# Kernel optimization log

Measured on AMD Instinct MI355X. Metric: run time of the kernel, lower is better.

The kernel has to match this reference:

```python
import jax, jax.numpy as jnp
import numpy as np

# Static per-expert capacities (tokens are laid out contiguously per expert)
CAPS = [1024, 512, 1024, 256, 1024, 512, 128, 1024, 512, 1024, 256, 512, 1024, 128, 64, 512]
TOTAL = sum(CAPS)  # 9536
E, H, I = 16, 1024, 4096
OFFSETS = np.concatenate([[0], np.cumsum(CAPS)])


def setup_inputs() -> dict:
    key = jax.random.key(0)
    ks = jax.random.split(key, 5)
    x = jax.random.normal(ks[0], (TOTAL, H), dtype=jnp.float32)
    W1 = jax.random.normal(ks[1], (E, I, H), dtype=jnp.float32) * 0.02
    b1 = jax.random.normal(ks[2], (E, I), dtype=jnp.float32) * 0.02
    W2 = jax.random.normal(ks[3], (E, H, I), dtype=jnp.float32) * 0.02
    b2 = jax.random.normal(ks[4], (E, H), dtype=jnp.float32) * 0.02
    return {"x": x, "W1": W1, "b1": b1, "W2": W2, "b2": b2}


def reference(x, W1, b1, W2, b2):
    # Grouped GEMM FFN: expert e processes rows [OFFSETS[e]:OFFSETS[e+1]]
    # out = gelu(x_e @ W1[e].T + b1[e]) @ W2[e].T + b2[e]
    outs = []
    for e in range(E):  # fixed, static loop over experts (capacities are static)
        xs = x[OFFSETS[e]:OFFSETS[e + 1]]                      # [cap_e, H]
        h = jax.nn.gelu(xs @ W1[e].T + b1[e], approximate=False)  # [cap_e, I]
        outs.append(h @ W2[e].T + b2[e])                       # [cap_e, H]
    return jnp.concatenate(outs, axis=0)                       # [TOTAL, H]
```

## Files before the change

kernel.cpp:

```cpp
#include <hip/hip_runtime.h>
#include <math.h>

typedef __attribute__((ext_vector_type(8))) short short8;
typedef __attribute__((ext_vector_type(4))) float f32x4;
typedef __attribute__((ext_vector_type(2))) unsigned int u32x2;

#define E_NUM 16
constexpr int CAPS[E_NUM] = {1024,512,1024,256,1024,512,128,1024,512,1024,256,512,1024,128,64,512};
constexpr int OFFS[E_NUM] = {0,1024,1536,2560,2816,3840,4352,4480,5504,6016,7040,7296,7808,8832,8960,9024};
constexpr int cdiv_(int a, int b){ return (a + b - 1) / b; }
constexpr int ilog2_(int v){ int l = 0; while ((1 << l) < v) ++l; return l; }

__device__ __forceinline__ unsigned int cvt_pk_bf16(float a, float b){
  unsigned int r;
  asm("v_cvt_pk_bf16_f32 %0, %1, %2" : "=v"(r) : "v"(a), "v"(b));
  return r;
}

typedef __attribute__((address_space(1))) const unsigned char gas_u8;
typedef __attribute__((address_space(3))) unsigned char las_u8;
__device__ __forceinline__ void gl_lds16(const void* g, void* l){
  __builtin_amdgcn_global_load_lds((gas_u8*)g, (las_u8*)l, 16, 0, 0);
}

__global__ __launch_bounds__(256) void cvt_bf16_kernel(const float* __restrict__ x,
                                                       unsigned short* __restrict__ xb, int n8)
{
  int i = blockIdx.x * blockDim.x + threadIdx.x;
  const int stride = gridDim.x * blockDim.x;
  for (; i < n8; i += stride) {
    f32x4 a = *reinterpret_cast<const f32x4*>(x + (size_t)i * 8);
    f32x4 b = *reinterpret_cast<const f32x4*>(x + (size_t)i * 8 + 4);
    u32x2 lo, hi;
    lo[0] = cvt_pk_bf16(a[0], a[1]); lo[1] = cvt_pk_bf16(a[2], a[3]);
    hi[0] = cvt_pk_bf16(b[0], b[1]); hi[1] = cvt_pk_bf16(b[2], b[3]);
    *reinterpret_cast<u32x2*>(xb + (size_t)i * 8)     = lo;
    *reinterpret_cast<u32x2*>(xb + (size_t)i * 8 + 4) = hi;
  }
}

template<bool A_GLDS, bool GELU_OUT, int TM, int NDIM, int KDIM, int LOG_GN, int NWG, int KS>
__global__ __launch_bounds__(256, 8)
void expert_gemm(const void* __restrict__ Av, const float* __restrict__ W,
                 const float* __restrict__ bias, void* __restrict__ Outv)
{
  constexpr int A_SZ = TM * 32;
  constexpr int B_SZ = 128 * 32;
  constexpr int GN   = 1 << LOG_GN;
  constexpr int MFR  = TM / 32;
  constexpr int NT   = KDIM / (KS * 32);
  constexpr int NWG1 = NWG / KS;
  static_assert(NWG % 8 == 0, "grid must be divisible by 8 for XCD swizzle");
  static_assert(!GELU_OUT || 2 * (A_SZ + B_SZ) >= 128 * 128, "GELU transpose needs 32KB");
  static_assert(!GELU_OUT || KS == 1, "GELU path is KS=1 only");

  __shared__ __align__(16) unsigned short smem[2 * A_SZ + 2 * B_SZ];

  const int tid  = threadIdx.x;
  const int braw = blockIdx.x;
  const int t = (braw & 7) * (NWG / 8) + (braw >> 3);

  const int kc    = t / NWG1;
  const int tt    = t % NWG1;
  const int kbase = kc * (KDIM / KS);

  int m0 = 0, n0 = 0, Me = 0, tok0 = 0;
  size_t wbase = 0, bbase = 0;
  {
    int acc0 = 0;
    #pragma unroll
    for (int i = 0; i < E_NUM; ++i) {
      const int mt  = cdiv_(CAPS[i], TM);
      const int lmt = ilog2_(mt);
      const int nb  = mt * (NDIM / 128);
      if (tt >= acc0 && tt < acc0 + nb) {
        const int loc = tt - acc0;
        const int g   = loc >> (lmt + LOG_GN);
        const int rem = loc & ((mt << LOG_GN) - 1);
        m0   = (rem >> LOG_GN) * TM;
        n0   = ((g << LOG_GN) | (rem & (GN - 1))) * 128;
        Me   = CAPS[i];
        tok0 = OFFS[i];
        wbase = (size_t)i * NDIM * KDIM;
        bbase = (size_t)i * NDIM;
      }
      acc0 += nb;
    }
  }
  const float* Wb = W + wbase;

  const int lane = tid & 63;
  const int wv   = tid >> 6;
  const int sr   = tid >> 3;
  const int sc   = (tid & 7) * 8;
  const int spc  = sc ^ (((sr >> 2) & 3) << 4);

  const unsigned short* Ah = (const unsigned short*)Av;
  const float*          Af = (const float*)Av;

  f32x4 ra[MFR]; f32x4 rb[4];

  auto loadB = [&](int kt) {
    const int k0 = kbase + kt * 32;
    #pragma unroll
    for (int i = 0; i < 4; ++i)
      rb[i] = *reinterpret_cast<const f32x4*>(Wb + (size_t)(n0 + sr + 32 * i) * KDIM + k0 + (sc >> 1));
  };
  auto writeB = [&](int buf) {
    char* bb = (char*)(smem + 2 * A_SZ + buf * B_SZ);
    #pragma unroll
    for (int i = 0; i < 4; ++i) {
      u32x2 p;
      p[0] = cvt_pk_bf16(rb[i][0], rb[i][1]);
      p[1] = cvt_pk_bf16(rb[i][2], rb[i][3]);
      *reinterpret_cast<u32x2*>(bb + (sr + 32 * i) * 64 + spc) = p;
    }
  };

  auto stageA_glds = [&](int buf, int kt) {
    constexpr int AI = TM / 64;
    const unsigned short* Ag = Ah + (size_t)(tok0 + m0) * KDIM + kbase + kt * 32;
    #pragma unroll
    for (int j = 0; j < AI; ++j) {
      const int rbase = wv * (AI * 16) + j * 16;
      const int r     = rbase + (lane >> 2);
      const int gblk  = (lane & 3) ^ ((r >> 2) & 3);
      gl_lds16((const void*)(Ag + (size_t)r * KDIM + gblk * 8),
               (void*)(smem + buf * A_SZ + rbase * 32));
    }
  };
  auto loadA_reg = [&](int kt) {
    const int k0 = kbase + kt * 32;
    #pragma unroll
    for (int i = 0; i < MFR; ++i)
      ra[i] = *reinterpret_cast<const f32x4*>(Af + (size_t)(tok0 + m0 + sr + 32 * i) * KDIM + k0 + (sc >> 1));
  };
  auto writeA_reg = [&](int buf) {
    char* ab = (char*)(smem + buf * A_SZ);
    #pragma unroll
    for (int i = 0; i < MFR; ++i) {
      u32x2 p;
      p[0] = cvt_pk_bf16(ra[i][0], ra[i][1]);
      p[1] = cvt_pk_bf16(ra[i][2], ra[i][3]);
      *reinterpret_cast<u32x2*>(ab + (sr + 32 * i) * 64 + spc) = p;
    }
  };

  const int wm   = (wv >> 1) * (TM / 2);
  const int wn   = (wv & 1) * 64;
  const int lrow = lane & 15;
  const int fcs  = ((lane >> 4) << 4) ^ (((lane >> 2) & 3) << 4);

  f32x4 acc_[MFR][4];
  #pragma unroll
  for (int i = 0; i < MFR; ++i)
    #pragma unroll
    for (int j = 0; j < 4; ++j)
      acc_[i][j] = (f32x4){0.f, 0.f, 0.f, 0.f};

  auto mfma_step = [&](int cur) {
    const char* ab = (const char*)(smem + cur * A_SZ);
    const char* bb = (const char*)(smem + 2 * A_SZ + cur * B_SZ);
    short8 afr[MFR], bfr[4];
    #pragma unroll
    for (int f = 0; f < MFR; ++f)
      afr[f] = *reinterpret_cast<const short8*>(ab + (wm + f * 16 + lrow) * 64 + fcs);
    #pragma unroll
    for (int f = 0; f < 4; ++f)
      bfr[f] = *reinterpret_cast<const short8*>(bb + (wn + f * 16 + lrow) * 64 + fcs);
    #pragma unroll
    for (int i = 0; i < MFR; ++i)
      #pragma unroll
      for (int j = 0; j < 4; ++j)
        acc_[i][j] = __builtin_amdgcn_mfma_f32_16x16x32_bf16(afr[i], bfr[j], acc_[i][j], 0, 0, 0);
  };

  loadB(0);
  if constexpr (A_GLDS) stageA_glds(0, 0); else loadA_reg(0);
  writeB(0);
  if constexpr (!A_GLDS) writeA_reg(0);
  __syncthreads();

  for (int kt = 0; kt < NT; ++kt) {
    const int cur = kt & 1;
    if (kt + 1 < NT) {
      loadB(kt + 1);
      if constexpr (A_GLDS) stageA_glds(cur ^ 1, kt + 1);
      else                  loadA_reg(kt + 1);
    }
    mfma_step(cur);
    if (kt + 1 < NT) {
      writeB(cur ^ 1);
      if constexpr (!A_GLDS) writeA_reg(cur ^ 1);
    }
    __syncthreads();
  }

  float bv[4];
  #pragma unroll
  for (int f = 0; f < 4; ++f)
    bv[f] = bias[bbase + n0 + wn + f * 16 + lrow];

  if constexpr (GELU_OUT) {
    static_assert(TM == 128, "GELU path assumes 128-row tiles");
    unsigned short* hout = smem;
    #pragma unroll
    for (int i = 0; i < MFR; ++i) {
      const int rbase = wm + i * 16 + (lane >> 4) * 4;
      #pragma unroll
      for (int j = 0; j < 4; ++j) {
        #pragma unroll
        for (int jj = 0; jj < 4; ++jj) {
          float xv = acc_[i][j][jj] + bv[j];
          float y2 = xv * (1.5957691216057308f + 0.07135481627f * xv * xv);
          float g  = xv * __builtin_amdgcn_rcpf(1.0f + __expf(-y2));
          hout[(rbase + jj) * 128 + wn + j * 16 + lrow] = (unsigned short)(cvt_pk_bf16(g, g) & 0xFFFFu);
        }
      }
    }
    __syncthreads();
    unsigned short* Oh = (unsigned short*)Outv;
    #pragma unroll
    for (int it = 0; it < 8; ++it) {
      int row  = it * 16 + (tid >> 4);
      int c    = (tid & 15) * 8;
      int grow = m0 + row;
      if (grow < Me) {
        *reinterpret_cast<short8*>(Oh + (size_t)(tok0 + grow) * NDIM + n0 + c)
          = *reinterpret_cast<const short8*>(hout + row * 128 + c);
      }
    }
  } else {
    float* Of = (float*)Outv;
    constexpr float BS = 1.0f / (float)KS;
    #pragma unroll
    for (int i = 0; i < MFR; ++i) {
      const int rbase = wm + i * 16 + (lane >> 4) * 4;
      #pragma unroll
      for (int jj = 0; jj < 4; ++jj) {
        int grow = m0 + rbase + jj;
        if (grow < Me) {
          #pragma unroll
          for (int j = 0; j < 4; ++j) {
            float v = acc_[i][j][jj] + bv[j] * BS;
            float* p = Of + (size_t)(tok0 + grow) * NDIM + n0 + wn + j * 16 + lrow;
            if constexpr (KS > 1) unsafeAtomicAdd(p, v);
            else                  *p = v;
          }
        }
      }
    }
  }
}

extern "C" void kernel_launch(void* const* d_in, const int* in_sizes, int n_in,
                              void* d_out, int out_size, void* d_ws, size_t ws_size,
                              hipStream_t stream)
{
  const float* x  = (const float*)d_in[0];
  const float* W1 = (const float*)d_in[1];
  const float* b1 = (const float*)d_in[2];
  const float* W2 = (const float*)d_in[3];
  const float* b2 = (const float*)d_in[4];
  float* out = (float*)d_out;

  constexpr size_t H_BYTES  = (size_t)9536 * 4096 * 2;
  constexpr size_t XB_BYTES = (size_t)9536 * 1024 * 2;
  unsigned short* h  = (unsigned short*)d_ws;
  unsigned short* xb = (unsigned short*)((char*)d_ws + H_BYTES);

  const bool use_xb = ws_size >= H_BYTES + XB_BYTES;

  hipMemsetAsync(d_out, 0, (size_t)out_size * sizeof(float), stream);

  if (use_xb) {
    cvt_bf16_kernel<<<2048, 256, 0, stream>>>(x, xb, 9536 * 1024 / 8);
    expert_gemm<true, true, 128, 4096, 1024, 2, 75 * 32, 1>
        <<<75 * 32, 256, 0, stream>>>((const void*)xb, W1, b1, (void*)h);
  } else {
    expert_gemm<false, true, 128, 4096, 1024, 2, 75 * 32, 1>
        <<<75 * 32, 256, 0, stream>>>((const void*)x, W1, b1, (void*)h);
  }

  expert_gemm<true, false, 128, 1024, 4096, 0, 2 * 75 * 8, 2>
      <<<2 * 75 * 8, 256, 0, stream>>>((const void*)h, W2, b2, (void*)out);
}
```

Measured before the change: 367.2 us.

## Stage fp32 weights directly to LDS and convert to bf16 at fragment load

Weight tiles are now copied from global memory into LDS as raw fp32 using the direct global-to-LDS load path, instead of being loaded into registers, converted to bf16 and written to LDS. Conversion to bf16 moves into the MFMA fragment read, with a new XOR swizzle for both A and B tiles. This frees registers and removes the register round-trip and its stalls. In exchange the B tile in LDS doubles in size, LDS reads per step double, the conversion is repeated by each wave reading the same tile, and the occupancy hint drops from 8 to 3 blocks.

Result: no change. 371.6 us (+1.2%).

```diff
diff --git a/kernel.cpp b/kernel.cpp
--- a/kernel.cpp
+++ b/kernel.cpp
@@ -4,6 +4,7 @@
 typedef __attribute__((ext_vector_type(8))) short short8;
 typedef __attribute__((ext_vector_type(4))) float f32x4;
 typedef __attribute__((ext_vector_type(2))) unsigned int u32x2;
+typedef __attribute__((ext_vector_type(4))) unsigned int u32x4;
 
 #define E_NUM 16
 constexpr int CAPS[E_NUM] = {1024,512,1024,256,1024,512,128,1024,512,1024,256,512,1024,128,64,512};
@@ -40,21 +41,21 @@
 }
 
 template<bool A_GLDS, bool GELU_OUT, int TM, int NDIM, int KDIM, int LOG_GN, int NWG, int KS>
-__global__ __launch_bounds__(256, 8)
+__global__ __launch_bounds__(256, 3)
 void expert_gemm(const void* __restrict__ Av, const float* __restrict__ W,
                  const float* __restrict__ bias, void* __restrict__ Outv)
 {
-  constexpr int A_SZ = TM * 32;
-  constexpr int B_SZ = 128 * 32;
+  constexpr int A_BYTES = TM * 64;
+  constexpr int B_BYTES = 128 * 128;
   constexpr int GN   = 1 << LOG_GN;
   constexpr int MFR  = TM / 32;
   constexpr int NT   = KDIM / (KS * 32);
   constexpr int NWG1 = NWG / KS;
   static_assert(NWG % 8 == 0, "grid must be divisible by 8 for XCD swizzle");
-  static_assert(!GELU_OUT || 2 * (A_SZ + B_SZ) >= 128 * 128, "GELU transpose needs 32KB");
+  static_assert(!GELU_OUT || (2 * A_BYTES + 2 * B_BYTES) >= 128 * 128 * 2, "GELU needs 32KB");
   static_assert(!GELU_OUT || KS == 1, "GELU path is KS=1 only");
 
-  __shared__ __align__(16) unsigned short smem[2 * A_SZ + 2 * B_SZ];
+  __shared__ __align__(16) char smem[2 * A_BYTES + 2 * B_BYTES];
 
   const int tid  = threadIdx.x;
   const int braw = blockIdx.x;
@@ -91,44 +92,37 @@
 
   const int lane = tid & 63;
   const int wv   = tid >> 6;
-  const int sr   = tid >> 3;
-  const int sc   = (tid & 7) * 8;
-  const int spc  = sc ^ (((sr >> 2) & 3) << 4);
 
   const unsigned short* Ah = (const unsigned short*)Av;
   const float*          Af = (const float*)Av;
 
-  f32x4 ra[MFR]; f32x4 rb[4];
-
-  auto loadB = [&](int kt) {
-    const int k0 = kbase + kt * 32;
-    #pragma unroll
-    for (int i = 0; i < 4; ++i)
-      rb[i] = *reinterpret_cast<const f32x4*>(Wb + (size_t)(n0 + sr + 32 * i) * KDIM + k0 + (sc >> 1));
-  };
-  auto writeB = [&](int buf) {
-    char* bb = (char*)(smem + 2 * A_SZ + buf * B_SZ);
-    #pragma unroll
-    for (int i = 0; i < 4; ++i) {
-      u32x2 p;
-      p[0] = cvt_pk_bf16(rb[i][0], rb[i][1]);
-      p[1] = cvt_pk_bf16(rb[i][2], rb[i][3]);
-      *reinterpret_cast<u32x2*>(bb + (sr + 32 * i) * 64 + spc) = p;
-    }
-  };
-
-  auto stageA_glds = [&](int buf, int kt) {
-    constexpr int AI = TM / 64;
+  auto stageB = [&](int buf, int kt) {
+    const float* Bg = Wb + (size_t)n0 * KDIM + kbase + kt * 32;
+    char* dst0 = smem + 2 * A_BYTES + buf * B_BYTES;
+    #pragma unroll
+    for (int j = 0; j < 4; ++j) {
+      const int rbase = wv * 32 + j * 8;
+      const int r     = rbase + (lane >> 3);
+      const int lblk  = (lane & 7) ^ (r & 7);
+      gl_lds16((const void*)(Bg + (size_t)r * KDIM + lblk * 4), (void*)(dst0 + rbase * 128));
+    }
+  };
+
+  auto stageA = [&](int buf, int kt) {
     const unsigned short* Ag = Ah + (size_t)(tok0 + m0) * KDIM + kbase + kt * 32;
-    #pragma unroll
-    for (int j = 0; j < AI; ++j) {
-      const int rbase = wv * (AI * 16) + j * 16;
+    char* dst0 = smem + buf * A_BYTES;
+    #pragma unroll
+    for (int j = 0; j < TM / 64; ++j) {
+      const int rbase = wv * (TM / 4) + j * 16;
       const int r     = rbase + (lane >> 2);
-      const int gblk  = (lane & 3) ^ ((r >> 2) & 3);
-      gl_lds16((const void*)(Ag + (size_t)r * KDIM + gblk * 8),
-               (void*)(smem + buf * A_SZ + rbase * 32));
-    }
-  };
+      const int lblk  = (lane & 3) ^ (r & 3);
+      gl_lds16((const void*)(Ag + (size_t)r * KDIM + lblk * 8), (void*)(dst0 + rbase * 64));
+    }
+  };
+
+  const int sr = tid >> 3;
+  const int sc = (tid & 7) * 8;
+  f32x4 ra[MFR];
   auto loadA_reg = [&](int kt) {
     const int k0 = kbase + kt * 32;
     #pragma unroll
@@ -136,20 +130,21 @@
       ra[i] = *reinterpret_cast<const f32x4*>(Af + (size_t)(tok0 + m0 + sr + 32 * i) * KDIM + k0 + (sc >> 1));
   };
   auto writeA_reg = [&](int buf) {
-    char* ab = (char*)(smem + buf * A_SZ);
+    char* ab = smem + buf * A_BYTES;
     #pragma unroll
     for (int i = 0; i < MFR; ++i) {
       u32x2 p;
       p[0] = cvt_pk_bf16(ra[i][0], ra[i][1]);
       p[1] = cvt_pk_bf16(ra[i][2], ra[i][3]);
-      *reinterpret_cast<u32x2*>(ab + (sr + 32 * i) * 64 + spc) = p;
+      *reinterpret_cast<u32x2*>(ab + (sr + 32 * i) * 64 + (sc ^ ((sr & 3) << 4))) = p;
     }
   };
 
   const int wm   = (wv >> 1) * (TM / 2);
   const int wn   = (wv & 1) * 64;
   const int lrow = lane & 15;
-  const int fcs  = ((lane >> 4) << 4) ^ (((lane >> 2) & 3) << 4);
+  const int pa0  = (((lane >> 4) ^ (lane & 3)) << 4);
+  const int pb0  = ((((lane >> 4) << 1) ^ (lane & 7)) << 4);
 
   f32x4 acc_[MFR][4];
   #pragma unroll
@@ -159,15 +154,24 @@
       acc_[i][j] = (f32x4){0.f, 0.f, 0.f, 0.f};
 
   auto mfma_step = [&](int cur) {
-    const char* ab = (const char*)(smem + cur * A_SZ);
-    const char* bb = (const char*)(smem + 2 * A_SZ + cur * B_SZ);
+    const char* ab  = smem + cur * A_BYTES;
+    const char* bbp = smem + 2 * A_BYTES + cur * B_BYTES;
     short8 afr[MFR], bfr[4];
     #pragma unroll
     for (int f = 0; f < MFR; ++f)
-      afr[f] = *reinterpret_cast<const short8*>(ab + (wm + f * 16 + lrow) * 64 + fcs);
-    #pragma unroll
-    for (int f = 0; f < 4; ++f)
-      bfr[f] = *reinterpret_cast<const short8*>(bb + (wn + f * 16 + lrow) * 64 + fcs);
+      afr[f] = *reinterpret_cast<const short8*>(ab + (wm + f * 16 + lrow) * 64 + pa0);
+    #pragma unroll
+    for (int f = 0; f < 4; ++f) {
+      const char* rowp = bbp + (size_t)(wn + f * 16 + lrow) * 128;
+      f32x4 lo = *reinterpret_cast<const f32x4*>(rowp + pb0);
+      f32x4 hi = *reinterpret_cast<const f32x4*>(rowp + (pb0 ^ 16));
+      u32x4 pk;
+      pk[0] = cvt_pk_bf16(lo[0], lo[1]);
+      pk[1] = cvt_pk_bf16(lo[2], lo[3]);
+      pk[2] = cvt_pk_bf16(hi[0], hi[1]);
+      pk[3] = cvt_pk_bf16(hi[2], hi[3]);
+      bfr[f] = __builtin_bit_cast(short8, pk);
+    }
     #pragma unroll
     for (int i = 0; i < MFR; ++i)
       #pragma unroll
@@ -175,24 +179,19 @@
         acc_[i][j] = __builtin_amdgcn_mfma_f32_16x16x32_bf16(afr[i], bfr[j], acc_[i][j], 0, 0, 0);
   };
 
-  loadB(0);
-  if constexpr (A_GLDS) stageA_glds(0, 0); else loadA_reg(0);
-  writeB(0);
-  if constexpr (!A_GLDS) writeA_reg(0);
+  if constexpr (A_GLDS) stageA(0, 0); else { loadA_reg(0); writeA_reg(0); }
+  stageB(0, 0);
   __syncthreads();
 
   for (int kt = 0; kt < NT; ++kt) {
     const int cur = kt & 1;
     if (kt + 1 < NT) {
-      loadB(kt + 1);
-      if constexpr (A_GLDS) stageA_glds(cur ^ 1, kt + 1);
+      stageB(cur ^ 1, kt + 1);
+      if constexpr (A_GLDS) stageA(cur ^ 1, kt + 1);
       else                  loadA_reg(kt + 1);
     }
     mfma_step(cur);
-    if (kt + 1 < NT) {
-      writeB(cur ^ 1);
-      if constexpr (!A_GLDS) writeA_reg(cur ^ 1);
-    }
+    if constexpr (!A_GLDS) { if (kt + 1 < NT) writeA_reg(cur ^ 1); }
     __syncthreads();
   }
 
@@ -203,7 +202,7 @@
 
   if constexpr (GELU_OUT) {
     static_assert(TM == 128, "GELU path assumes 128-row tiles");
-    unsigned short* hout = smem;
+    unsigned short* hout = (unsigned short*)smem;
     #pragma unroll
     for (int i = 0; i < MFR; ++i) {
       const int rbase = wm + i * 16 + (lane >> 4) * 4;
```
